# Optimization experiments

Measured on AMD Instinct MI355X. Metric: run time of the kernel, lower is better.

Reference implementation:

```python
import jax, jax.numpy as jnp
import numpy as np

B, T = 4096, 256
COND, INTV, H = 128, 64, 256


def _glorot(key, shape):
    fan_in = shape[0]
    return jax.random.normal(key, shape, dtype=jnp.float32) / np.sqrt(fan_in)


def setup_inputs() -> dict:
    key = jax.random.key(0)
    ks = jax.random.split(key, 20)
    inp = {
        "cond": jax.random.normal(ks[0], (B, COND), dtype=jnp.float32),
        "interval_feat": jax.random.normal(ks[1], (B, INTV), dtype=jnp.float32),
        "times": jnp.cumsum(jax.random.uniform(ks[2], (B, T), dtype=jnp.float32), axis=1),
        "seq_lens": jax.random.randint(ks[3], (B,), 1, T + 1),
        # seq_feature MLP: INTV -> 2*INTV -> 2*INTV -> INTV
        "w1": _glorot(ks[4], (INTV, 2 * INTV)), "b1": jnp.zeros((2 * INTV,), jnp.float32),
        "w2": _glorot(ks[5], (2 * INTV, 2 * INTV)), "b2": jnp.zeros((2 * INTV,), jnp.float32),
        "w3": _glorot(ks[6], (2 * INTV, INTV)), "b3": jnp.zeros((INTV,), jnp.float32),
        # h0 projection: (COND+INTV) -> H
        "w_h0": _glorot(ks[7], (COND + INTV, H)), "b_h0": jnp.zeros((H,), jnp.float32),
        # GRUCell (input dim 1), gate order r,z,n
        "w_ih": _glorot(ks[8], (1, 3 * H)), "b_ih": jnp.zeros((3 * H,), jnp.float32),
        "w_hh": _glorot(ks[9], (H, 3 * H)), "b_hh": jnp.zeros((3 * H,), jnp.float32),
        # head: H -> 2 (delta, stop logit)
        "w_head": _glorot(ks[10], (H, 2)), "b_head": jnp.zeros((2,), jnp.float32),
    }
    return inp


def reference(cond, interval_feat, times, seq_lens,
              w1, b1, w2, b2, w3, b3, w_h0, b_h0,
              w_ih, w_hh, b_ih, b_hh, w_head, b_head):
    # seq_feature MLP
    s = jax.nn.relu(interval_feat @ w1 + b1)
    s = jax.nn.relu(s @ w2 + b2)
    seq_emb = s @ w3 + b3
    # initial hidden state
    h0 = jnp.tanh(jnp.concatenate([cond, seq_emb], axis=-1) @ w_h0 + b_h0)  # (B,H)
    # ground-truth deltas; step 0 input is 0, step i>=1 input is gt_delta[:, i-1]
    gt_delta = jnp.diff(times, axis=1, prepend=jnp.zeros((times.shape[0], 1), times.dtype))  # (B,T)
    xs = jnp.concatenate([jnp.zeros((1, times.shape[0]), times.dtype), gt_delta.T], axis=0)  # (T+1,B)

    def step(h, x):
        gi = x[:, None] * w_ih[0] + b_ih          # (B,3H)
        gh = h @ w_hh + b_hh                       # (B,3H)
        gi_r, gi_z, gi_n = jnp.split(gi, 3, axis=-1)
        gh_r, gh_z, gh_n = jnp.split(gh, 3, axis=-1)
        r = jax.nn.sigmoid(gi_r + gh_r)
        z = jax.nn.sigmoid(gi_z + gh_z)
        n = jnp.tanh(gi_n + r * gh_n)
        h_new = (1.0 - z) * n + z * h
        out = h_new @ w_head + b_head              # (B,2)
        return h_new, out

    _, outs = jax.lax.scan(step, h0, xs)           # outs: (T+1,B,2)
    pred_delta = outs[:, :, 0].T                   # (B,T+1)
    stop_logits = outs[:, :, 1].T                  # (B,T+1)
    return pred_delta, stop_logits
```

## Files before the change

### kernel.cpp

```cpp
#include <hip/hip_runtime.h>
#include <cstddef>

typedef _Float16 f16x8 __attribute__((ext_vector_type(8)));
typedef float    f32x4 __attribute__((ext_vector_type(4)));

#define Bc 4096
#define Tc 256
#define NSTEP 257
#define RB 16
#define HSTR 264
#define HEAD_OFF 393216

__device__ inline float sigm(float x)  { return __builtin_amdgcn_rcpf(1.f + __expf(-x)); }
__device__ inline float tanh_(float x) { return 1.f - 2.f * __builtin_amdgcn_rcpf(1.f + __expf(2.f * x)); }

__global__ __launch_bounds__(256) void build_frags(
    const float* __restrict__ w_hh, const float* __restrict__ w_head,
    _Float16* __restrict__ ws)
{
    int flat = blockIdx.x * 256 + threadIdx.x;
    if (blockIdx.x < 96) {
        int f    = flat >> 6;
        int lane = flat & 63;
        int kt   = f & 7;
        int nc   = (f >> 3) % 3;
        int trio = f / 24;
        int c     = nc * 256 + trio * 16 + (lane & 15);
        int kbase = kt * 32 + (lane >> 4) * 8;
        _Float16* dst = ws + (size_t)f * 512 + (size_t)lane * 8;
        #pragma unroll
        for (int j = 0; j < 8; ++j)
            dst[j] = (_Float16)w_hh[(size_t)(kbase + j) * 768 + c];
    } else {
        int idx = flat - 96 * 256;
        int kt   = idx >> 6;
        int lane = idx & 63;
        int col   = lane & 15;
        int kbase = kt * 32 + (lane >> 4) * 8;
        _Float16* dst = ws + HEAD_OFF / 2 + (size_t)kt * 512 + (size_t)lane * 8;
        #pragma unroll
        for (int j = 0; j < 8; ++j)
            dst[j] = (col < 2) ? (_Float16)w_head[(size_t)(kbase + j) * 2 + col]
                               : (_Float16)0.f;
    }
}

__global__ __attribute__((amdgpu_waves_per_eu(2, 2))) __launch_bounds__(512)
void gru_mfma(
    const float* __restrict__ cond, const float* __restrict__ ivf,
    const float* __restrict__ times,
    const float* __restrict__ w1, const float* __restrict__ b1,
    const float* __restrict__ w2, const float* __restrict__ b2,
    const float* __restrict__ w3, const float* __restrict__ b3,
    const float* __restrict__ wh0, const float* __restrict__ bh0,
    const float* __restrict__ w_ih, const float* __restrict__ b_ih,
    const float* __restrict__ b_hh, const float* __restrict__ b_head,
    const _Float16* __restrict__ wfrag,
    float* __restrict__ out)
{
    __shared__ __align__(16) _Float16 h16[RB * HSTR];
    __shared__ float  xs[RB * NSTEP];
    __shared__ __align__(16) _Float16 headB[4096];
    __shared__ float  gateC[256 * 8];
    __shared__ float  outbuf[2][RB][16];
    __shared__ float  bh2[2];
    __shared__ float  mlp1[RB * 128];
    __shared__ float  mlp2[RB * 128];
    __shared__ float  embS[RB * 64];
    __shared__ float  h0f[RB * 256];

    const int tid  = threadIdx.x;
    const int w    = tid >> 6;
    const int lane = tid & 63;
    const int l15  = lane & 15;
    const int q    = lane >> 4;
    const int row0 = blockIdx.x * RB;

    for (int o = tid; o < RB * 128; o += 512) {
        int r = o >> 7, c = o & 127;
        float a = b1[c];
        #pragma unroll 4
        for (int k = 0; k < 64; ++k)
            a = fmaf(ivf[(size_t)(row0 + r) * 64 + k], w1[k * 128 + c], a);
        mlp1[o] = fmaxf(a, 0.f);
    }
    __syncthreads();
    for (int o = tid; o < RB * 128; o += 512) {
        int r = o >> 7, c = o & 127;
        float a = b2[c];
        #pragma unroll 4
        for (int k = 0; k < 128; ++k)
            a = fmaf(mlp1[r * 128 + k], w2[k * 128 + c], a);
        mlp2[o] = fmaxf(a, 0.f);
    }
    __syncthreads();
    for (int o = tid; o < RB * 64; o += 512) {
        int r = o >> 6, c = o & 63;
        float a = b3[c];
        #pragma unroll 4
        for (int k = 0; k < 128; ++k)
            a = fmaf(mlp2[r * 128 + k], w3[k * 64 + c], a);
        embS[o] = a;
    }
    __syncthreads();
    for (int o = tid; o < RB * 256; o += 512) {
        int r = o >> 8, c = o & 255;
        float a = bh0[c];
        #pragma unroll 4
        for (int k = 0; k < 128; ++k)
            a = fmaf(cond[(size_t)(row0 + r) * 128 + k], wh0[k * 256 + c], a);
        #pragma unroll 4
        for (int k = 0; k < 64; ++k)
            a = fmaf(embS[r * 64 + k], wh0[(128 + k) * 256 + c], a);
        h0f[o] = tanh_(a);
    }
    __syncthreads();

    for (int o = tid; o < RB * 256; o += 512) {
        int r = o >> 8, c = o & 255;
        h16[r * HSTR + c] = (_Float16)h0f[o];
    }
    for (int o = tid; o < RB * NSTEP; o += 512) {
        int r = o / NSTEP, ii = o - r * NSTEP;
        float x = 0.f;
        if (ii >= 1) {
            float a = times[(size_t)(row0 + r) * Tc + (ii - 1)];
            float b = (ii >= 2) ? times[(size_t)(row0 + r) * Tc + (ii - 2)] : 0.f;
            x = a - b;
        }
        xs[o] = x;
    }
    {
        const float4* src = (const float4*)(wfrag + HEAD_OFF / 2);
        ((float4*)headB)[tid] = src[tid];
    }
    for (int uu = tid; uu < 256; uu += 512) {
        gateC[uu * 8 + 0] = w_ih[uu];
        gateC[uu * 8 + 1] = w_ih[256 + uu];
        gateC[uu * 8 + 2] = w_ih[512 + uu];
        gateC[uu * 8 + 3] = b_ih[uu] + b_hh[uu];
        gateC[uu * 8 + 4] = b_ih[256 + uu] + b_hh[256 + uu];
        gateC[uu * 8 + 5] = b_ih[512 + uu];
        gateC[uu * 8 + 6] = b_hh[512 + uu];
        gateC[uu * 8 + 7] = 0.f;
    }
    if (tid < 2) bh2[tid] = b_head[tid];

    const int u0 = w * 32 + l15;
    const int u1 = u0 + 16;

    f16x8 Bf[2][3][8];
    #pragma unroll
    for (int p = 0; p < 2; ++p)
        #pragma unroll
        for (int nc = 0; nc < 3; ++nc)
            #pragma unroll
            for (int kt = 0; kt < 8; ++kt)
                Bf[p][nc][kt] = *(const f16x8*)(wfrag
                    + (size_t)(((2 * w + p) * 3 + nc) * 8 + kt) * 512
                    + (size_t)lane * 8);

    __syncthreads();

    float hold[2][4];
    #pragma unroll
    for (int p = 0; p < 2; ++p)
        #pragma unroll
        for (int j = 0; j < 4; ++j)
            hold[p][j] = h0f[(q * 4 + j) * 256 + (p ? u1 : u0)];

    for (int i = 0; i <= NSTEP; ++i) {
        const bool doGh   = (i < NSTEP);
        const bool doHead = (i >= 1) && (w == 0);

        f32x4 aR[2], aZ[2], aN[2];
        #pragma unroll
        for (int p = 0; p < 2; ++p) {
            aR[p] = (f32x4){0.f, 0.f, 0.f, 0.f};
            aZ[p] = (f32x4){0.f, 0.f, 0.f, 0.f};
            aN[p] = (f32x4){0.f, 0.f, 0.f, 0.f};
        }
        f32x4 aH = (f32x4){0.f, 0.f, 0.f, 0.f};

        #pragma unroll
        for (int kt = 0; kt < 8; ++kt) {
            f16x8 Af = *(const f16x8*)(h16 + l15 * HSTR + kt * 32 + q * 8);
            if (doGh) {
                #pragma unroll
                for (int p = 0; p < 2; ++p) {
                    aR[p] = __builtin_amdgcn_mfma_f32_16x16x32_f16(Af, Bf[p][0][kt], aR[p], 0, 0, 0);
                    aZ[p] = __builtin_amdgcn_mfma_f32_16x16x32_f16(Af, Bf[p][1][kt], aZ[p], 0, 0, 0);
                    aN[p] = __builtin_amdgcn_mfma_f32_16x16x32_f16(Af, Bf[p][2][kt], aN[p], 0, 0, 0);
                }
            }
            if (doHead) {
                f16x8 Bh = *(const f16x8*)(headB + kt * 512 + lane * 8);
                aH = __builtin_amdgcn_mfma_f32_16x16x32_f16(Af, Bh, aH, 0, 0, 0);
            }
        }

        if (doHead && l15 < 2) {
            const int o = i - 1;
            #pragma unroll
            for (int j = 0; j < 4; ++j)
                outbuf[l15][q * 4 + j][o & 15] = aH[j];
        }

        __syncthreads();

        if (i >= 1) {
            const int o = i - 1;
            if (((o & 15) == 15) || (o == NSTEP - 1)) {
                const int cnt   = (o & 15) + 1;
                const int obase = o & ~15;
                const int e     = tid & 15;
                const int row   = (tid >> 4) & 15;
                const int plane = tid >> 8;
                if (e < cnt)
                    out[(size_t)plane * ((size_t)Bc * NSTEP)
                        + (size_t)(row0 + row) * NSTEP + obase + e]
                        = outbuf[plane][row][e] + bh2[plane];
            }
        }

        if (doGh) {
            #pragma unroll
            for (int p = 0; p < 2; ++p) {
                const int u = p ? u1 : u0;
                const f32x4 g0 = *(const f32x4*)(gateC + u * 8);
                const f32x4 g1 = *(const f32x4*)(gateC + u * 8 + 4);
                #pragma unroll
                for (int j = 0; j < 4; ++j) {
                    const int m = q * 4 + j;
                    const float x  = xs[m * NSTEP + i];
                    const float rr = sigm(fmaf(x, g0[0], g0[3]) + aR[p][j]);
                    const float zz = sigm(fmaf(x, g0[1], g1[0]) + aZ[p][j]);
                    const float nn = tanh_(fmaf(x, g0[2], g1[1]) + rr * (aN[p][j] + g1[2]));
                    const float hn = nn + zz * (hold[p][j] - nn);
                    hold[p][j] = hn;
                    h16[m * HSTR + u] = (_Float16)hn;
                }
            }
        }
        __syncthreads();
    }
}

extern "C" void kernel_launch(void* const* d_in, const int* in_sizes, int n_in,
                              void* d_out, int out_size, void* d_ws, size_t ws_size,
                              hipStream_t stream) {
    const float* cond   = (const float*)d_in[0];
    const float* ivf    = (const float*)d_in[1];
    const float* times  = (const float*)d_in[2];
    const float* w1     = (const float*)d_in[4];
    const float* b1     = (const float*)d_in[5];
    const float* w2     = (const float*)d_in[6];
    const float* b2     = (const float*)d_in[7];
    const float* w3     = (const float*)d_in[8];
    const float* b3     = (const float*)d_in[9];
    const float* wh0    = (const float*)d_in[10];
    const float* bh0    = (const float*)d_in[11];
    const float* w_ih   = (const float*)d_in[12];
    const float* b_ih   = (const float*)d_in[13];
    const float* w_hh   = (const float*)d_in[14];
    const float* b_hh   = (const float*)d_in[15];
    const float* w_head = (const float*)d_in[16];
    const float* b_head = (const float*)d_in[17];

    float*    outp = (float*)d_out;
    _Float16* ws   = (_Float16*)d_ws;

    build_frags<<<98, 256, 0, stream>>>(w_hh, w_head, ws);
    gru_mfma<<<Bc / RB, 512, 0, stream>>>(cond, ivf, times,
                                          w1, b1, w2, b2, w3, b3, wh0, bh0,
                                          w_ih, b_ih, b_hh, b_head,
                                          (const _Float16*)ws, outp);
}
```

Measured before the change: 718.2 us.

## Double-buffer GRU hidden state to drop one barrier per timestep

Splits the shared-memory hidden state into two ping-pong buffers, so each step reads one buffer and writes the other. This removes the mid-step __syncthreads that separated the MFMA reads of h from the gate update writes. The output-head flush now runs entirely in wave 0, which avoids needing a barrier between the outbuf writes and the global stores. It also raises wave priority around the MFMA loop; the cost is extra LDS for the second buffer and more serial store work in wave 0.

```diff
diff --git a/kernel.cpp b/kernel.cpp
--- a/kernel.cpp
+++ b/kernel.cpp
@@ -58,7 +58,8 @@
     const _Float16* __restrict__ wfrag,
     float* __restrict__ out)
 {
-    __shared__ __align__(16) _Float16 h16[RB * HSTR];
+    __shared__ __align__(16) _Float16 hA[RB * HSTR];
+    __shared__ __align__(16) _Float16 hB[RB * HSTR];
     __shared__ float  xs[RB * NSTEP];
     __shared__ __align__(16) _Float16 headB[4096];
     __shared__ float  gateC[256 * 8];
@@ -118,7 +119,7 @@
 
     for (int o = tid; o < RB * 256; o += 512) {
         int r = o >> 8, c = o & 255;
-        h16[r * HSTR + c] = (_Float16)h0f[o];
+        hA[r * HSTR + c] = (_Float16)h0f[o];
     }
     for (int o = tid; o < RB * NSTEP; o += 512) {
         int r = o / NSTEP, ii = o - r * NSTEP;
@@ -169,9 +170,9 @@
         for (int j = 0; j < 4; ++j)
             hold[p][j] = h0f[(q * 4 + j) * 256 + (p ? u1 : u0)];
 
-    for (int i = 0; i <= NSTEP; ++i) {
-        const bool doGh   = (i < NSTEP);
-        const bool doHead = (i >= 1) && (w == 0);
+    auto STEP = [&](const _Float16* hc, _Float16* hn, int i) {
+        const bool doGh = (i < NSTEP);
+        const bool doHd = (i >= 1) && (w == 0);
 
         f32x4 aR[2], aZ[2], aN[2];
         #pragma unroll
@@ -182,44 +183,48 @@
         }
         f32x4 aH = (f32x4){0.f, 0.f, 0.f, 0.f};
 
+        __builtin_amdgcn_s_setprio(1);
         #pragma unroll
         for (int kt = 0; kt < 8; ++kt) {
-            f16x8 Af = *(const f16x8*)(h16 + l15 * HSTR + kt * 32 + q * 8);
-            if (doGh) {
+            if (doGh || doHd) {
+                f16x8 Af = *(const f16x8*)(hc + l15 * HSTR + kt * 32 + q * 8);
+                if (doGh) {
+                    #pragma unroll
+                    for (int p = 0; p < 2; ++p) {
+                        aR[p] = __builtin_amdgcn_mfma_f32_16x16x32_f16(Af, Bf[p][0][kt], aR[p], 0, 0, 0);
+                        aZ[p] = __builtin_amdgcn_mfma_f32_16x16x32_f16(Af, Bf[p][1][kt], aZ[p], 0, 0, 0);
+                        aN[p] = __builtin_amdgcn_mfma_f32_16x16x32_f16(Af, Bf[p][2][kt], aN[p], 0, 0, 0);
+                    }
+                }
+                if (doHd) {
+                    f16x8 Bh = *(const f16x8*)(headB + kt * 512 + lane * 8);
+                    aH = __builtin_amdgcn_mfma_f32_16x16x32_f16(Af, Bh, aH, 0, 0, 0);
+                }
+            }
+        }
+        __builtin_amdgcn_s_setprio(0);
+
+        if (doHd) {
+            const int o = i - 1;
+            if (l15 < 2) {
                 #pragma unroll
-                for (int p = 0; p < 2; ++p) {
-                    aR[p] = __builtin_amdgcn_mfma_f32_16x16x32_f16(Af, Bf[p][0][kt], aR[p], 0, 0, 0);
-                    aZ[p] = __builtin_amdgcn_mfma_f32_16x16x32_f16(Af, Bf[p][1][kt], aZ[p], 0, 0, 0);
-                    aN[p] = __builtin_amdgcn_mfma_f32_16x16x32_f16(Af, Bf[p][2][kt], aN[p], 0, 0, 0);
-                }
-            }
-            if (doHead) {
-                f16x8 Bh = *(const f16x8*)(headB + kt * 512 + lane * 8);
-                aH = __builtin_amdgcn_mfma_f32_16x16x32_f16(Af, Bh, aH, 0, 0, 0);
-            }
-        }
-
-        if (doHead && l15 < 2) {
-            const int o = i - 1;
-            #pragma unroll
-            for (int j = 0; j < 4; ++j)
-                outbuf[l15][q * 4 + j][o & 15] = aH[j];
-        }
-
-        __syncthreads();
-
-        if (i >= 1) {
-            const int o = i - 1;
+                for (int j = 0; j < 4; ++j)
+                    outbuf[l15][q * 4 + j][o & 15] = aH[j];
+            }
             if (((o & 15) == 15) || (o == NSTEP - 1)) {
                 const int cnt   = (o & 15) + 1;
                 const int obase = o & ~15;
-                const int e     = tid & 15;
-                const int row   = (tid >> 4) & 15;
-                const int plane = tid >> 8;
-                if (e < cnt)
-                    out[(size_t)plane * ((size_t)Bc * NSTEP)
-                        + (size_t)(row0 + row) * NSTEP + obase + e]
-                        = outbuf[plane][row][e] + bh2[plane];
+                #pragma unroll
+                for (int s = 0; s < 8; ++s) {
+                    const int idx   = s * 64 + lane;
+                    const int e     = idx & 15;
+                    const int row   = (idx >> 4) & 15;
+                    const int plane = idx >> 8;
+                    if (e < cnt)
+                        out[(size_t)plane * ((size_t)Bc * NSTEP)
+                            + (size_t)(row0 + row) * NSTEP + obase + e]
+                            = outbuf[plane][row][e] + bh2[plane];
+                }
             }
         }
 
@@ -236,13 +241,18 @@
                     const float rr = sigm(fmaf(x, g0[0], g0[3]) + aR[p][j]);
                     const float zz = sigm(fmaf(x, g0[1], g1[0]) + aZ[p][j]);
                     const float nn = tanh_(fmaf(x, g0[2], g1[1]) + rr * (aN[p][j] + g1[2]));
-                    const float hn = nn + zz * (hold[p][j] - nn);
-                    hold[p][j] = hn;
-                    h16[m * HSTR + u] = (_Float16)hn;
+                    const float hn_ = nn + zz * (hold[p][j] - nn);
+                    hold[p][j] = hn_;
+                    hn[m * HSTR + u] = (_Float16)hn_;
                 }
             }
         }
         __syncthreads();
+    };
+
+    for (int i = 0; i < NSTEP + 1; i += 2) {
+        STEP(hA, hB, i);
+        STEP(hB, hA, i + 1);
     }
 }
 
```

Measured after the change: 849.8 us. +18.3%, slower.
